# Performance work log

Measured on AMD Instinct MI355X. Metric: run time of the kernel, lower is better.

## Reference

```python
import jax, jax.numpy as jnp
import numpy as np

S, D_IN, D_OUT = 4096, 1024, 1024

def setup_inputs() -> dict:
    key = jax.random.key(0)
    kx, kq, kk, kv = jax.random.split(key, 4)
    scale = 0.02
    return {
        "x": jax.random.normal(kx, (S, D_IN), dtype=jnp.float32),
        "W_query": jax.random.normal(kq, (D_IN, D_OUT), dtype=jnp.float32) * scale,
        "W_key": jax.random.normal(kk, (D_IN, D_OUT), dtype=jnp.float32) * scale,
        "W_value": jax.random.normal(kv, (D_IN, D_OUT), dtype=jnp.float32) * scale,
    }

def reference(x, W_query, W_key, W_value):
    # x: [S, d_in]; W_*: [d_in, d_out]
    queries = x @ W_query        # [S, d_out]
    keys = x @ W_key             # [S, d_out]
    values = x @ W_value         # [S, d_out]
    d_k = keys.shape[-1]
    attn_scores = queries @ keys.T            # [S, S]
    attn_weights = jax.nn.softmax(attn_scores / jnp.sqrt(jnp.float32(d_k)), axis=-1)
    context_vec = attn_weights @ values       # [S, d_out]
    return context_vec
```

## Files before the change

### kernel.cpp

```cpp
#include <hip/hip_runtime.h>

typedef _Float16 f16x8 __attribute__((ext_vector_type(8)));
typedef float f32x4 __attribute__((ext_vector_type(4)));
typedef unsigned short u16;
typedef u16 u16x8 __attribute__((ext_vector_type(8)));
typedef u16 u16x4 __attribute__((ext_vector_type(4)));

__device__ __forceinline__ u16 f2h_bits(float f) {
    _Float16 h = (_Float16)f;
    return __builtin_bit_cast(u16, h);
}
__device__ __forceinline__ float h2f(u16 b) {
    return (float)__builtin_bit_cast(_Float16, b);
}

typedef __attribute__((address_space(1))) unsigned int gu32_as1;
typedef __attribute__((address_space(3))) unsigned int lu32_as3;
__device__ __forceinline__ void gload16(const u16* g, u16* l) {
    __builtin_amdgcn_global_load_lds((gu32_as1*)g, (lu32_as3*)l, 16, 0, 0);
}

#define BAR   __builtin_amdgcn_s_barrier()
#define LGK0  asm volatile("s_waitcnt lgkmcnt(0)" ::: "memory")
#define VM6   asm volatile("s_waitcnt vmcnt(6)" ::: "memory")
#define VM0   asm volatile("s_waitcnt vmcnt(0)" ::: "memory")
#define PRIO1 __builtin_amdgcn_s_setprio(1)
#define PRIO0 __builtin_amdgcn_s_setprio(0)

template <int MODE>
__global__ __launch_bounds__(512, 2) void gemm_bt(
    const u16* __restrict__ A, int lda,
    const u16* __restrict__ B, int ldb,
    u16* __restrict__ C, int ldc,
    int Ksplit, float alpha, size_t c_z_stride,
    int bnW, int bmW, int numPanelX,
    float* __restrict__ rowsum, u16* __restrict__ vt,
    float* __restrict__ outF)
{
    __shared__ __attribute__((aligned(16))) u16 As[32768];
    __shared__ __attribute__((aligned(16))) u16 Bs[32768];

    const int t    = threadIdx.x;
    const int lane = t & 63;
    const int wave = t >> 6;
    const int wm   = wave >> 2;
    const int wn   = wave & 3;
    const int l16  = lane & 15;
    const int quad = lane >> 4;

    const int lin = blockIdx.y * gridDim.x + blockIdx.x;
    const int xcd = lin & 7;
    const int idx = lin >> 3;
    const int px  = xcd % numPanelX;
    const int py  = xcd / numPanelX;
    const int bn  = px * bnW + idx % bnW;
    const int bm  = py * bmW + idx / bnW;

    const int kz = blockIdx.z;
    A += (size_t)kz * Ksplit;
    B += (size_t)kz * Ksplit;
    if (MODE != 3) C += (size_t)kz * c_z_stride;

    const int srow = t >> 3;
    const int sseg = ((t & 7) ^ ((t >> 3) & 7)) * 8;
    const u16* Ag = A + (size_t)(bm * 256 + srow) * lda + sseg;
    const u16* Bg = B + (size_t)(bn * 256 + srow) * ldb + sseg;
    u16* AsD = &As[t * 8];
    u16* BsD = &Bs[t * 8];

#define STG_A(h, bufv, kt) do {                                         \
        const u16* _s = Ag + (size_t)(h) * 128 * lda + (size_t)(kt) * 64; \
        u16* _d = AsD + (bufv) * 16384 + (h) * 8192;                    \
        gload16(_s, _d);                                                \
        gload16(_s + (size_t)64 * lda, _d + 4096);                      \
    } while (0)
#define STG_B(h, bufv, kt) do {                                         \
        const u16* _s = Bg + (size_t)(h) * 128 * ldb + (size_t)(kt) * 64; \
        u16* _d = BsD + (bufv) * 16384 + (h) * 8192;                    \
        gload16(_s, _d);                                                \
        gload16(_s + (size_t)64 * ldb, _d + 4096);                      \
    } while (0)

    const int skz = l16 & 7;
    const int sk0 = (quad ^ skz) * 8;
    const int sk1 = ((4 + quad) ^ skz) * 8;
    const u16* Ab = As + wm * 8192 + l16 * 64;
    const u16* Bb = Bs + (wn >> 1) * 8192 + (wn & 1) * 4096 + l16 * 64;

#define RD_A(dst, mh, bufv) do {                                        \
        _Pragma("unroll") for (int mi = 0; mi < 4; mi++) {              \
            dst[mi][0] = *(const f16x8*)(Ab + (bufv) * 16384 +          \
                                         (mh) * 4096 + mi * 1024 + sk0);\
            dst[mi][1] = *(const f16x8*)(Ab + (bufv) * 16384 +          \
                                         (mh) * 4096 + mi * 1024 + sk1);\
        } } while (0)
#define RD_B(dst, nh, bufv) do {                                        \
        _Pragma("unroll") for (int nj = 0; nj < 2; nj++) {              \
            dst[nj][0] = *(const f16x8*)(Bb + (bufv) * 16384 +          \
                                         (nh) * 2048 + nj * 1024 + sk0);\
            dst[nj][1] = *(const f16x8*)(Bb + (bufv) * 16384 +          \
                                         (nh) * 2048 + nj * 1024 + sk1);\
        } } while (0)
#define MFQ(mh, nh, Af, Bf) do {                                        \
        _Pragma("unroll") for (int mi = 0; mi < 4; mi++)                \
        _Pragma("unroll") for (int nj = 0; nj < 2; nj++)                \
        _Pragma("unroll") for (int kk = 0; kk < 2; kk++)                \
            acc[(mh)*4+mi][(nh)*2+nj] =                                 \
                __builtin_amdgcn_mfma_f32_16x16x32_f16(                 \
                    Af[mi][kk], Bf[nj][kk], acc[(mh)*4+mi][(nh)*2+nj],  \
                    0, 0, 0);                                           \
    } while (0)

    f32x4 acc[8][4] = {};
    const int NI = Ksplit >> 7;

    STG_A(0, 0, 0); STG_A(1, 0, 0); STG_B(0, 0, 0); STG_B(1, 0, 0);
    STG_B(0, 1, 1); STG_A(0, 1, 1); STG_B(1, 1, 1);
    VM6;
    BAR;

    for (int it = 0; it < NI; ++it) {
        const int t0 = it * 2, t1 = it * 2 + 1;
        const bool nl = (it + 1 < NI);
        f16x8 a0[4][2], a1[4][2], b0[2][2], b1[2][2];

        RD_A(a0, 0, 0); RD_B(b0, 0, 0);
        STG_A(1, 1, t1);
        BAR; LGK0; PRIO1; MFQ(0, 0, a0, b0); PRIO0; BAR;
        RD_B(b1, 1, 0);
        if (nl) STG_B(0, 0, t0 + 2);
        BAR; LGK0; PRIO1; MFQ(0, 1, a0, b1); PRIO0; BAR;
        RD_A(a1, 1, 0);
        if (nl) STG_A(0, 0, t0 + 2);
        BAR; LGK0; PRIO1; MFQ(1, 0, a1, b0); PRIO0; BAR;
        if (nl) STG_B(1, 0, t0 + 2);
        BAR; LGK0; PRIO1; MFQ(1, 1, a1, b1); PRIO0;
        if (nl) VM6; else VM0;
        BAR;
        RD_A(a0, 0, 1); RD_B(b0, 0, 1);
        if (nl) STG_A(1, 0, t0 + 2);
        BAR; LGK0; PRIO1; MFQ(0, 0, a0, b0); PRIO0; BAR;
        RD_B(b1, 1, 1);
        if (nl) STG_B(0, 1, t1 + 2);
        BAR; LGK0; PRIO1; MFQ(0, 1, a0, b1); PRIO0; BAR;
        RD_A(a1, 1, 1);
        if (nl) STG_A(0, 1, t1 + 2);
        BAR; LGK0; PRIO1; MFQ(1, 0, a1, b0); PRIO0; BAR;
        if (nl) STG_B(1, 1, t1 + 2);
        BAR; LGK0; PRIO1; MFQ(1, 1, a1, b1); PRIO0;
        if (nl) VM6; else VM0;
        BAR;
    }
#undef STG_A
#undef STG_B
#undef RD_A
#undef RD_B
#undef MFQ

    const int crow = bm * 256 + wm * 128 + quad * 4;
    const int ccol = bn * 256 + wn * 64 + l16;

    if (MODE == 1) {
        float rs[8][4];
#pragma unroll
        for (int mi = 0; mi < 8; mi++)
#pragma unroll
            for (int r = 0; r < 4; r++) rs[mi][r] = 0.f;
#pragma unroll
        for (int mi = 0; mi < 8; mi++) {
#pragma unroll
            for (int ni = 0; ni < 4; ni++) {
#pragma unroll
                for (int r = 0; r < 4; r++) {
                    float e = __expf(acc[mi][ni][r] * alpha);
                    rs[mi][r] += e;
                    C[(size_t)(crow + mi * 16 + r) * ldc + (ccol + ni * 16)] = f2h_bits(e);
                }
            }
        }
#pragma unroll
        for (int mi = 0; mi < 8; mi++) {
#pragma unroll
            for (int r = 0; r < 4; r++) {
                float s = rs[mi][r];
#pragma unroll
                for (int o = 1; o < 16; o <<= 1) s += __shfl_xor(s, o);
                if (l16 == 0)
                    atomicAdd(&rowsum[crow + mi * 16 + r], s);
            }
        }
    } else if (MODE == 2 && bn >= 8) {
#pragma unroll
        for (int ni = 0; ni < 4; ni++) {
            const int cV = (bn - 8) * 256 + wn * 64 + ni * 16 + l16;
#pragma unroll
            for (int mi = 0; mi < 8; mi++) {
                u16x4 o;
#pragma unroll
                for (int r = 0; r < 4; r++) o[r] = f2h_bits(acc[mi][ni][r]);
                *(u16x4*)(vt + (size_t)cV * 4096 + crow + mi * 16) = o;
            }
        }
    } else if (MODE == 3) {
#pragma unroll
        for (int mi = 0; mi < 8; mi++) {
#pragma unroll
            for (int r = 0; r < 4; r++) {
                const int row = crow + mi * 16 + r;
                const float inv = 1.0f / rowsum[row];
#pragma unroll
                for (int ni = 0; ni < 4; ni++)
                    atomicAdd(&outF[(size_t)row * ldc + (ccol + ni * 16)],
                              acc[mi][ni][r] * inv);
            }
        }
    } else {
#pragma unroll
        for (int mi = 0; mi < 8; mi++)
#pragma unroll
            for (int ni = 0; ni < 4; ni++)
#pragma unroll
                for (int r = 0; r < 4; r++)
                    C[(size_t)(crow + mi * 16 + r) * ldc + (ccol + ni * 16)] =
                        f2h_bits(acc[mi][ni][r] * alpha);
    }
}

__global__ __launch_bounds__(256) void prep(
    const float* __restrict__ x, u16* __restrict__ xb,
    const float* __restrict__ W0, const float* __restrict__ W1,
    const float* __restrict__ W2, u16* __restrict__ Wt,
    float* __restrict__ lr)
{
    __shared__ float tile[32][33];
    const int bid = blockIdx.x;
    const int t   = threadIdx.x;

    if (bid < 4096) {
        int i = (bid * 256 + t) * 4;
        float4 v = *(const float4*)(x + i);
        ushort4 o;
        o.x = f2h_bits(v.x);
        o.y = f2h_bits(v.y);
        o.z = f2h_bits(v.z);
        o.w = f2h_bits(v.w);
        *(ushort4*)(xb + i) = o;
    } else if (bid < 4096 + 3072) {
        const int b   = bid - 4096;
        const int z   = b >> 10;
        const int rem = b & 1023;
        const float* in = (z == 0) ? W0 : (z == 1) ? W1 : W2;
        u16* o = Wt + (size_t)z * 1024 * 1024;
        const int bx = (rem & 31) * 32;
        const int by = (rem >> 5) * 32;
        const int tx = t & 31, ty = t >> 5;
#pragma unroll
        for (int j = 0; j < 4; j++)
            tile[ty + j * 8][tx] = in[(size_t)(by + ty + j * 8) * 1024 + bx + tx];
        __syncthreads();
#pragma unroll
        for (int j = 0; j < 4; j++)
            o[(size_t)(bx + ty + j * 8) * 1024 + by + tx] = f2h_bits(tile[tx][ty + j * 8]);
    } else {
        int i = ((bid - 4096 - 3072) * 256 + t) * 4;
        *(float4*)(lr + i) = float4{0.f, 0.f, 0.f, 0.f};
    }
}

extern "C" void kernel_launch(void* const* d_in, const int* in_sizes, int n_in,
                              void* d_out, int out_size, void* d_ws, size_t ws_size,
                              hipStream_t stream)
{
    (void)in_sizes; (void)n_in; (void)out_size; (void)ws_size;
    const float* x  = (const float*)d_in[0];
    const float* Wq = (const float*)d_in[1];
    const float* Wk = (const float*)d_in[2];
    const float* Wv = (const float*)d_in[3];
    float* out = (float*)d_out;
    char* ws = (char*)d_ws;

    u16* xb  = (u16*)(ws);
    u16* Wt  = (u16*)(ws + ((size_t)8  << 20));
    u16* QK  = (u16*)(ws + ((size_t)14 << 20));
    u16* Sb  = (u16*)(ws + ((size_t)32 << 20));
    u16* Vt  = (u16*)(ws + ((size_t)64 << 20));
    float* lr = (float*)(ws + ((size_t)72 << 20));

    const int S = 4096, D = 1024;

    prep<<<4096 + 3072 + 4, 256, 0, stream>>>(x, xb, Wq, Wk, Wv, Wt, lr);

    hipMemsetAsync(out, 0, (size_t)S * D * sizeof(float), stream);

    gemm_bt<2><<<dim3(12, 16, 1), 512, 0, stream>>>(
        xb, D, Wt, D, QK, 2048, D, 1.0f, 0, 3, 8, 4, nullptr, Vt, nullptr);

    gemm_bt<1><<<dim3(16, 16, 1), 512, 0, stream>>>(
        QK, 2048, QK + 1024, 2048, Sb, S, D, 0.03125f, 0, 4, 8, 4, lr, nullptr,
        nullptr);

    gemm_bt<3><<<dim3(4, 16, 4), 512, 0, stream>>>(
        Sb, S, Vt, S, nullptr, D, 1024, 1.0f, 0, 1, 8, 4, lr, nullptr, out);
}
```

Baseline: 249.4 us.

## Replace split-K atomic accumulation with last-block reduction of fp16 partials

The final P·V GEMM used split-K with fp32 atomicAdd into a zeroed output, which needed a separate memset. Each split now writes its partial tile in fp16 to a workspace buffer and bumps a per-tile counter. The block that arrives last sums the other three partials plus its own accumulator, normalizes by the row sum, and stores the result once. This drops the memset and the atomic traffic on the output, at the cost of extra partial-buffer writes and reads, fp16 rounding of the partials, and a serialized tail on the last block per tile.

```diff
diff --git a/kernel.cpp b/kernel.cpp
--- a/kernel.cpp
+++ b/kernel.cpp
@@ -35,7 +35,7 @@
     int Ksplit, float alpha, size_t c_z_stride,
     int bnW, int bmW, int numPanelX,
     float* __restrict__ rowsum, u16* __restrict__ vt,
-    float* __restrict__ outF)
+    float* __restrict__ outF, unsigned int* __restrict__ cnt)
 {
     __shared__ __attribute__((aligned(16))) u16 As[32768];
     __shared__ __attribute__((aligned(16))) u16 Bs[32768];
@@ -59,7 +59,7 @@
     const int kz = blockIdx.z;
     A += (size_t)kz * Ksplit;
     B += (size_t)kz * Ksplit;
-    if (MODE != 3) C += (size_t)kz * c_z_stride;
+    if (MODE != 4) C += (size_t)kz * c_z_stride;
 
     const int srow = t >> 3;
     const int sseg = ((t & 7) ^ ((t >> 3) & 7)) * 8;
@@ -201,17 +201,42 @@
                 *(u16x4*)(vt + (size_t)cV * 4096 + crow + mi * 16) = o;
             }
         }
-    } else if (MODE == 3) {
-#pragma unroll
-        for (int mi = 0; mi < 8; mi++) {
-#pragma unroll
-            for (int r = 0; r < 4; r++) {
-                const int row = crow + mi * 16 + r;
-                const float inv = 1.0f / rowsum[row];
-#pragma unroll
-                for (int ni = 0; ni < 4; ni++)
-                    atomicAdd(&outF[(size_t)row * ldc + (ccol + ni * 16)],
-                              acc[mi][ni][r] * inv);
+    } else if (MODE == 4) {
+        u16* Pown = C + (size_t)kz * c_z_stride;
+#pragma unroll
+        for (int mi = 0; mi < 8; mi++)
+#pragma unroll
+            for (int ni = 0; ni < 4; ni++)
+#pragma unroll
+                for (int r = 0; r < 4; r++)
+                    Pown[(size_t)(crow + mi * 16 + r) * ldc + (ccol + ni * 16)] =
+                        f2h_bits(acc[mi][ni][r]);
+        __threadfence();
+        __syncthreads();
+        int* flag = (int*)As;
+        if (t == 0)
+            flag[0] = (atomicAdd(&cnt[bm * 4 + bn], 1u) == 3u) ? 1 : 0;
+        __syncthreads();
+        if (flag[0]) {
+            __threadfence();
+#pragma unroll
+            for (int mi = 0; mi < 8; mi++) {
+#pragma unroll
+                for (int r = 0; r < 4; r++) {
+                    const int row = crow + mi * 16 + r;
+                    const float inv = 1.0f / rowsum[row];
+#pragma unroll
+                    for (int ni = 0; ni < 4; ni++) {
+                        const int col = ccol + ni * 16;
+                        float s = acc[mi][ni][r];
+#pragma unroll
+                        for (int z = 0; z < 4; z++)
+                            if (z != kz)
+                                s += h2f(C[(size_t)z * c_z_stride +
+                                           (size_t)row * ldc + col]);
+                        outF[(size_t)row * ldc + col] = s * inv;
+                    }
+                }
             }
         }
     } else {
@@ -230,7 +255,7 @@
     const float* __restrict__ x, u16* __restrict__ xb,
     const float* __restrict__ W0, const float* __restrict__ W1,
     const float* __restrict__ W2, u16* __restrict__ Wt,
-    float* __restrict__ lr)
+    float* __restrict__ lr, unsigned int* __restrict__ cnt)
 {
     __shared__ float tile[32][33];
     const int bid = blockIdx.x;
@@ -262,8 +287,10 @@
         for (int j = 0; j < 4; j++)
             o[(size_t)(bx + ty + j * 8) * 1024 + by + tx] = f2h_bits(tile[tx][ty + j * 8]);
     } else {
-        int i = ((bid - 4096 - 3072) * 256 + t) * 4;
+        const int zb = bid - 4096 - 3072;
+        int i = (zb * 256 + t) * 4;
         *(float4*)(lr + i) = float4{0.f, 0.f, 0.f, 0.f};
+        if (zb == 0 && t < 64) cnt[t] = 0u;
     }
 }
 
@@ -285,20 +312,22 @@
     u16* Sb  = (u16*)(ws + ((size_t)32 << 20));
     u16* Vt  = (u16*)(ws + ((size_t)64 << 20));
     float* lr = (float*)(ws + ((size_t)72 << 20));
+    unsigned int* cnt = (unsigned int*)(ws + ((size_t)72 << 20) + 16384);
+    u16* P   = (u16*)(ws);
 
     const int S = 4096, D = 1024;
 
-    prep<<<4096 + 3072 + 4, 256, 0, stream>>>(x, xb, Wq, Wk, Wv, Wt, lr);
-
-    hipMemsetAsync(out, 0, (size_t)S * D * sizeof(float), stream);
+    prep<<<4096 + 3072 + 4, 256, 0, stream>>>(x, xb, Wq, Wk, Wv, Wt, lr, cnt);
 
     gemm_bt<2><<<dim3(12, 16, 1), 512, 0, stream>>>(
-        xb, D, Wt, D, QK, 2048, D, 1.0f, 0, 3, 8, 4, nullptr, Vt, nullptr);
+        xb, D, Wt, D, QK, 2048, D, 1.0f, 0, 3, 8, 4, nullptr, Vt,
+        nullptr, nullptr);
 
     gemm_bt<1><<<dim3(16, 16, 1), 512, 0, stream>>>(
         QK, 2048, QK + 1024, 2048, Sb, S, D, 0.03125f, 0, 4, 8, 4, lr, nullptr,
-        nullptr);
-
-    gemm_bt<3><<<dim3(4, 16, 4), 512, 0, stream>>>(
-        Sb, S, Vt, S, nullptr, D, 1024, 1.0f, 0, 1, 8, 4, lr, nullptr, out);
-}
+        nullptr, nullptr);
+
+    gemm_bt<4><<<dim3(4, 16, 4), 512, 0, stream>>>(
+        Sb, S, Vt, S, P, D, 1024, 1.0f, (size_t)S * D, 1, 8, 4, lr, nullptr,
+        out, cnt);
+}
```

New measurement: 368.9 us. 48.0% more time.
